# Kernel tuning notes

Hardware: AMD Instinct MI355X
Metric: run time of the kernel (lower is better)

## Reference

```python
import jax, jax.numpy as jnp
import numpy as np

N, T = 512, 48
VOCAB, EMBED, HIDDEN, IMG_DIM = 32000, 1024, 1024, 4096


def setup_inputs() -> dict:
    key = jax.random.key(0)
    ks = jax.random.split(key, 12)
    s = 0.02
    return {
        "questions": jax.random.randint(ks[0], (N, T), 0, VOCAB, dtype=jnp.int32),
        "img_features": jax.random.normal(ks[1], (N, IMG_DIM), dtype=jnp.float32),
        "emb": jax.random.normal(ks[2], (VOCAB, EMBED), dtype=jnp.float32) * s,
        "W_img": jax.random.normal(ks[3], (HIDDEN, IMG_DIM), dtype=jnp.float32) * s,
        "b_img": jnp.zeros((HIDDEN,), dtype=jnp.float32),
        "W_ih": jax.random.normal(ks[4], (4 * HIDDEN, EMBED), dtype=jnp.float32) * s,
        "W_hh": jax.random.normal(ks[5], (4 * HIDDEN, HIDDEN), dtype=jnp.float32) * s,
        "b_ih": jnp.zeros((4 * HIDDEN,), dtype=jnp.float32),
        "b_hh": jnp.zeros((4 * HIDDEN,), dtype=jnp.float32),
        "W_out": jax.random.normal(ks[6], (VOCAB, HIDDEN), dtype=jnp.float32) * s,
        "b_out": jnp.zeros((VOCAB,), dtype=jnp.float32),
        "first_words": 1,
    }


def reference(questions, img_features, emb, W_img, b_img, W_ih, W_hh, b_ih, b_hh,
              W_out, b_out, first_words):
    H = W_hh.shape[1]
    n = questions.shape[0]
    emb_q = emb[questions].transpose(1, 0, 2)          # [T, N, E]
    emb_i = img_features @ W_img.T + b_img             # [N, H]
    if first_words:
        seq = jnp.concatenate([emb_i[None], emb_q], axis=0)   # [T+1, N, E]
    else:
        seq = jnp.concatenate([emb_q, emb_i[None]], axis=0)

    def cell(carry, x_t):
        h, c = carry
        gates = x_t @ W_ih.T + b_ih + h @ W_hh.T + b_hh   # [N, 4H]
        i, f, g, o = jnp.split(gates, 4, axis=-1)          # torch LSTMCell gate order
        i, f, o = jax.nn.sigmoid(i), jax.nn.sigmoid(f), jax.nn.sigmoid(o)
        g = jnp.tanh(g)
        c = f * c + i * g
        h = o * jnp.tanh(c)
        return (h, c), h

    h0 = jnp.zeros((n, H), dtype=seq.dtype)
    (_, _), hs = jax.lax.scan(cell, (h0, h0), seq)     # hs: [T+1, N, H]
    hidden_states = hs.transpose(1, 0, 2)              # [N, T+1, H]
    output = hidden_states[:, -1, :] @ W_out.T + b_out  # [N, vocab]
    return output, hidden_states
```

## Files before the change

kernel.cpp:

```cpp
#include <hip/hip_runtime.h>
#include <hip/hip_bf16.h>
#include <stdint.h>

typedef __bf16 bf16_t;
typedef __attribute__((ext_vector_type(8))) __bf16 bf16x8;
typedef __attribute__((ext_vector_type(4))) __bf16 bf16x4;
typedef __attribute__((ext_vector_type(4))) float f32x4;
#define LL long long

__device__ __forceinline__ void gl_lds16(const bf16_t* g, bf16_t* s) {
  __builtin_amdgcn_global_load_lds(
      (const __attribute__((address_space(1))) void*)g,
      (__attribute__((address_space(3))) void*)s, 16, 0, 0);
}

__device__ __forceinline__ float sigm(float x) {
  return 1.0f / (1.0f + __expf(-x));
}
__device__ __forceinline__ float tanh_s(float x) {
  float e = __expf(-2.0f * fabsf(x));
  float t = (1.0f - e) / (1.0f + e);
  return copysignf(t, x);
}

template<int BM, int OUTBF>
__global__ __launch_bounds__(256, 2)
void gemm_bt(const bf16_t* __restrict__ A, const bf16_t* __restrict__ B,
             const float* __restrict__ bias,
             bf16_t* __restrict__ Cb, float* __restrict__ Cf,
             int N, int K, const int* __restrict__ fw, LL off0, LL off1) {
  __shared__ bf16_t lds_a[BM * 32];
  __shared__ bf16_t lds_b[128 * 32];
  const int tid = threadIdx.x;
  const int w = tid >> 6, l = tid & 63;
  const LL m0 = (LL)blockIdx.x * BM;
  const LL n0 = (LL)blockIdx.y * 128;
  constexpr int MI = BM / 32;
  const int wm = w & 1, wn = w >> 1;
  f32x4 acc[MI][4] = {};

  const int srow = l >> 2;
  const int scol = (l & 3) * 8;

  for (int kt = 0; kt < K; kt += 32) {
    for (int c = w; c < BM / 16; c += 4)
      gl_lds16(A + (m0 + c * 16 + srow) * K + kt + scol, &lds_a[c * 512]);
#pragma unroll
    for (int j = 0; j < 2; ++j) {
      int c = w * 2 + j;
      gl_lds16(B + (n0 + c * 16 + srow) * K + kt + scol, &lds_b[c * 512]);
    }
    __syncthreads();
    const int fr = l & 15, fk = (l >> 4) * 8;
    bf16x8 af[MI], bfr[4];
#pragma unroll
    for (int i = 0; i < MI; ++i)
      af[i] = *(const bf16x8*)&lds_a[(wm * (BM / 2) + i * 16 + fr) * 32 + fk];
#pragma unroll
    for (int j = 0; j < 4; ++j)
      bfr[j] = *(const bf16x8*)&lds_b[(wn * 64 + j * 16 + fr) * 32 + fk];
#pragma unroll
    for (int i = 0; i < MI; ++i)
#pragma unroll
      for (int j = 0; j < 4; ++j)
        acc[i][j] = __builtin_amdgcn_mfma_f32_16x16x32_bf16(af[i], bfr[j],
                                                            acc[i][j], 0, 0, 0);
    __syncthreads();
  }

  const LL coff = (fw[0] ? off1 : off0);
  const int er = (l >> 4) * 4, ec = l & 15;
#pragma unroll
  for (int i = 0; i < MI; ++i) {
#pragma unroll
    for (int j = 0; j < 4; ++j) {
      LL mrow = m0 + wm * (BM / 2) + i * 16 + er;
      LL ncol = n0 + wn * 64 + j * 16 + ec;
      float bs = bias[ncol];
#pragma unroll
      for (int r = 0; r < 4; ++r) {
        float v = acc[i][j][r] + bs;
        if (OUTBF) Cb[coff + (mrow + r) * N + ncol] = (bf16_t)v;
        else       Cf[(mrow + r) * N + ncol] = v;
      }
    }
  }
}

__global__ __launch_bounds__(256, 2)
void lstm_step(const bf16_t* __restrict__ h_in, const bf16_t* __restrict__ Whh,
               const bf16_t* __restrict__ Gt, float* __restrict__ c,
               bf16_t* __restrict__ h_out, float* __restrict__ hid, int t) {
  __shared__ bf16_t lds_a[64 * 32];
  __shared__ bf16_t lds_b[128 * 32];
  __shared__ float lds_ex[64 * 128];
  const int tid = threadIdx.x;
  const int w = tid >> 6, l = tid & 63;
  const int m0 = blockIdx.x * 64;
  const int n0 = blockIdx.y * 128;
  const int wm = w & 1, wn = w >> 1;
  f32x4 acc[2][4] = {};
  const int srow = l >> 2, scol = (l & 3) * 8;

  for (int kt = 0; kt < 1024; kt += 32) {
    gl_lds16(h_in + (LL)(m0 + w * 16 + srow) * 1024 + kt + scol,
             &lds_a[w * 512]);
#pragma unroll
    for (int j = 0; j < 2; ++j) {
      int ch = w * 2 + j;
      gl_lds16(Whh + (LL)(n0 + ch * 16 + srow) * 1024 + kt + scol,
               &lds_b[ch * 512]);
    }
    __syncthreads();
    const int fr = l & 15, fk = (l >> 4) * 8;
    bf16x8 af[2], bfr[4];
#pragma unroll
    for (int i = 0; i < 2; ++i)
      af[i] = *(const bf16x8*)&lds_a[(wm * 32 + i * 16 + fr) * 32 + fk];
#pragma unroll
    for (int j = 0; j < 4; ++j)
      bfr[j] = *(const bf16x8*)&lds_b[(wn * 64 + j * 16 + fr) * 32 + fk];
#pragma unroll
    for (int i = 0; i < 2; ++i)
#pragma unroll
      for (int j = 0; j < 4; ++j)
        acc[i][j] = __builtin_amdgcn_mfma_f32_16x16x32_bf16(af[i], bfr[j],
                                                            acc[i][j], 0, 0, 0);
    __syncthreads();
  }

  const int er = (l >> 4) * 4, ec = l & 15;
#pragma unroll
  for (int i = 0; i < 2; ++i)
#pragma unroll
    for (int j = 0; j < 4; ++j)
#pragma unroll
      for (int r = 0; r < 4; ++r)
        lds_ex[(wm * 32 + i * 16 + er + r) * 128 + wn * 64 + j * 16 + ec] =
            acc[i][j][r];
  __syncthreads();

  for (int cidx = tid; cidx < 2048; cidx += 256) {
    int ml = cidx >> 5, jl = cidx & 31;
    int m = m0 + ml;
    int j = (n0 >> 2) + jl;
    float4 ge = *(const float4*)&lds_ex[ml * 128 + jl * 4];
    bf16x4 g4 = *(const bf16x4*)(Gt + (LL)m * 4096 + n0 + jl * 4);
    float gi = ge.x + (float)g4[0];
    float gf = ge.y + (float)g4[1];
    float gg = ge.z + (float)g4[2];
    float go = ge.w + (float)g4[3];
    float iv = sigm(gi), fv = sigm(gf), gv = tanh_s(gg), ov = sigm(go);
    LL cij = (LL)m * 1024 + j;
    float cn = fv * c[cij] + iv * gv;
    float hn = ov * tanh_s(cn);
    c[cij] = cn;
    h_out[cij] = (bf16_t)hn;
    hid[((LL)m * 49 + t) * 1024 + j] = hn;
  }
}

__global__ __launch_bounds__(256)
void cvt_f2b(const float* __restrict__ src, bf16_t* __restrict__ dst, LL n4) {
  LL i = (LL)blockIdx.x * blockDim.x + threadIdx.x;
  LL stride = (LL)gridDim.x * blockDim.x;
  for (; i < n4; i += stride) {
    float4 v = *(const float4*)(src + i * 4);
    bf16x4 o;
    o[0] = (bf16_t)v.x; o[1] = (bf16_t)v.y; o[2] = (bf16_t)v.z; o[3] = (bf16_t)v.w;
    *(bf16x4*)(dst + i * 4) = o;
  }
}

__global__ __launch_bounds__(256)
void permute_w(const float* __restrict__ W, bf16_t* __restrict__ Wp) {
  int p = blockIdx.x;
  int r = (p & 3) * 1024 + (p >> 2);
  float4 v = *(const float4*)(W + (LL)r * 1024 + threadIdx.x * 4);
  bf16x4 o;
  o[0] = (bf16_t)v.x; o[1] = (bf16_t)v.y; o[2] = (bf16_t)v.z; o[3] = (bf16_t)v.w;
  *(bf16x4*)(Wp + (LL)p * 1024 + threadIdx.x * 4) = o;
}

__global__ __launch_bounds__(256)
void bias_comb(const float* __restrict__ bih, const float* __restrict__ bhh,
               float* __restrict__ bp) {
  int p = blockIdx.x * blockDim.x + threadIdx.x;
  int r = (p & 3) * 1024 + (p >> 2);
  bp[p] = bih[r] + bhh[r];
}

__global__ __launch_bounds__(256)
void gather_emb(const int* __restrict__ q, const float* __restrict__ emb,
                bf16_t* __restrict__ Xb, const int* __restrict__ fw) {
  int b = blockIdx.x;
  int tq = b >> 9;
  int n = b & 511;
  int slot = fw[0] ? tq + 1 : tq;
  int row = q[n * 48 + tq];
  float4 v = *(const float4*)(emb + (LL)row * 1024 + threadIdx.x * 4);
  bf16x4 o;
  o[0] = (bf16_t)v.x; o[1] = (bf16_t)v.y; o[2] = (bf16_t)v.z; o[3] = (bf16_t)v.w;
  *(bf16x4*)(Xb + ((LL)slot * 512 + n) * 1024 + threadIdx.x * 4) = o;
}

extern "C" void kernel_launch(void* const* d_in, const int* in_sizes, int n_in,
                              void* d_out, int out_size, void* d_ws,
                              size_t ws_size, hipStream_t stream) {
  const int*   questions = (const int*)  d_in[0];
  const float* img       = (const float*)d_in[1];
  const float* emb       = (const float*)d_in[2];
  const float* W_img     = (const float*)d_in[3];
  const float* b_img     = (const float*)d_in[4];
  const float* W_ih      = (const float*)d_in[5];
  const float* W_hh      = (const float*)d_in[6];
  const float* b_ih      = (const float*)d_in[7];
  const float* b_hh      = (const float*)d_in[8];
  const float* W_out     = (const float*)d_in[9];
  const float* b_out     = (const float*)d_in[10];
  const int*   fw        = (const int*)  d_in[11];

  char* ws = (char*)d_ws;
  size_t off = 0;
  auto alloc = [&](size_t bytes) {
    char* p = ws + off;
    off += (bytes + 255) & ~(size_t)255;
    return p;
  };
  bf16_t* Xb    = (bf16_t*)alloc((size_t)49 * 512 * 1024 * 2);
  bf16_t* G     = (bf16_t*)alloc((size_t)49 * 512 * 4096 * 2);
  bf16_t* Wp_ih = (bf16_t*)alloc((size_t)4096 * 1024 * 2);
  bf16_t* Wp_hh = (bf16_t*)alloc((size_t)4096 * 1024 * 2);
  bf16_t* Woutb = (bf16_t*)alloc((size_t)32000 * 1024 * 2);
  bf16_t* Wimgb = (bf16_t*)alloc((size_t)1024 * 4096 * 2);
  bf16_t* imgb  = (bf16_t*)alloc((size_t)512 * 4096 * 2);
  float*  biasp = (float*) alloc((size_t)4096 * 4);
  bf16_t* h0    = (bf16_t*)alloc((size_t)512 * 1024 * 2);
  bf16_t* h1    = (bf16_t*)alloc((size_t)512 * 1024 * 2);
  float*  cbuf  = (float*) alloc((size_t)512 * 1024 * 4);

  float* out0 = (float*)d_out;
  float* hid  = out0 + (size_t)512 * 32000;

  hipMemsetAsync(h0, 0, (size_t)512 * 1024 * 2, stream);
  hipMemsetAsync(cbuf, 0, (size_t)512 * 1024 * 4, stream);

  cvt_f2b<<<dim3(2048), dim3(256), 0, stream>>>(W_out, Woutb, (LL)32000 * 1024 / 4);
  cvt_f2b<<<dim3(1024), dim3(256), 0, stream>>>(W_img, Wimgb, (LL)1024 * 4096 / 4);
  cvt_f2b<<<dim3(512),  dim3(256), 0, stream>>>(img,   imgb,  (LL)512 * 4096 / 4);
  permute_w<<<dim3(4096), dim3(256), 0, stream>>>(W_ih, Wp_ih);
  permute_w<<<dim3(4096), dim3(256), 0, stream>>>(W_hh, Wp_hh);
  bias_comb<<<dim3(16), dim3(256), 0, stream>>>(b_ih, b_hh, biasp);
  gather_emb<<<dim3(48 * 512), dim3(256), 0, stream>>>(questions, emb, Xb, fw);

  gemm_bt<64, 1><<<dim3(8, 8), dim3(256), 0, stream>>>(
      imgb, Wimgb, b_img, Xb, nullptr, 1024, 4096, fw,
      (LL)48 * 512 * 1024, (LL)0);

  gemm_bt<128, 1><<<dim3(196, 32), dim3(256), 0, stream>>>(
      Xb, Wp_ih, biasp, G, nullptr, 4096, 1024, fw, 0, 0);

  for (int t = 0; t < 49; ++t) {
    const bf16_t* hin = (t & 1) ? h1 : h0;
    bf16_t* hout = (t & 1) ? h0 : h1;
    lstm_step<<<dim3(8, 32), dim3(256), 0, stream>>>(
        hin, Wp_hh, G + (LL)t * 512 * 4096, cbuf, hout, hid, t);
  }

  gemm_bt<128, 0><<<dim3(4, 250), dim3(256), 0, stream>>>(
      h1, Woutb, b_out, nullptr, out0, 32000, 1024, fw, 0, 0);
}
```

Before: 1.919 ms.

## Replace per-step LSTM launches with persistent kernel holding W_hh slices in LDS

The 49 separate lstm_step launches become one persistent kernel with a 64x4 grid. Each block keeps a 16-unit slice of all four gates of W_hh resident in 128KB of swizzled LDS and holds the cell state in registers. Timesteps are separated by a per-row-tile atomic counter barrier. This removes launch overhead, the per-step reload of W_hh, and the global round trips for c, but it needs all 256 blocks co-resident (otherwise the spin barrier deadlocks) and it serialises on the cross-block barrier.

```diff
diff --git a/kernel.cpp b/kernel.cpp
--- a/kernel.cpp
+++ b/kernel.cpp
@@ -6,6 +6,7 @@
 typedef __attribute__((ext_vector_type(8))) __bf16 bf16x8;
 typedef __attribute__((ext_vector_type(4))) __bf16 bf16x4;
 typedef __attribute__((ext_vector_type(4))) float f32x4;
+typedef __attribute__((ext_vector_type(16))) float f32x16;
 #define LL long long
 
 __device__ __forceinline__ void gl_lds16(const bf16_t* g, bf16_t* s) {
@@ -87,76 +88,100 @@
   }
 }
 
-__global__ __launch_bounds__(256, 2)
-void lstm_step(const bf16_t* __restrict__ h_in, const bf16_t* __restrict__ Whh,
-               const bf16_t* __restrict__ Gt, float* __restrict__ c,
-               bf16_t* __restrict__ h_out, float* __restrict__ hid, int t) {
-  __shared__ bf16_t lds_a[64 * 32];
-  __shared__ bf16_t lds_b[128 * 32];
-  __shared__ float lds_ex[64 * 128];
-  const int tid = threadIdx.x;
-  const int w = tid >> 6, l = tid & 63;
-  const int m0 = blockIdx.x * 64;
-  const int n0 = blockIdx.y * 128;
-  const int wm = w & 1, wn = w >> 1;
-  f32x4 acc[2][4] = {};
-  const int srow = l >> 2, scol = (l & 3) * 8;
-
-  for (int kt = 0; kt < 1024; kt += 32) {
-    gl_lds16(h_in + (LL)(m0 + w * 16 + srow) * 1024 + kt + scol,
-             &lds_a[w * 512]);
-#pragma unroll
-    for (int j = 0; j < 2; ++j) {
-      int ch = w * 2 + j;
-      gl_lds16(Whh + (LL)(n0 + ch * 16 + srow) * 1024 + kt + scol,
-               &lds_b[ch * 512]);
-    }
-    __syncthreads();
-    const int fr = l & 15, fk = (l >> 4) * 8;
-    bf16x8 af[2], bfr[4];
-#pragma unroll
-    for (int i = 0; i < 2; ++i)
-      af[i] = *(const bf16x8*)&lds_a[(wm * 32 + i * 16 + fr) * 32 + fk];
-#pragma unroll
-    for (int j = 0; j < 4; ++j)
-      bfr[j] = *(const bf16x8*)&lds_b[(wn * 64 + j * 16 + fr) * 32 + fk];
-#pragma unroll
-    for (int i = 0; i < 2; ++i)
-#pragma unroll
-      for (int j = 0; j < 4; ++j)
-        acc[i][j] = __builtin_amdgcn_mfma_f32_16x16x32_bf16(af[i], bfr[j],
-                                                            acc[i][j], 0, 0, 0);
-    __syncthreads();
-  }
-
-  const int er = (l >> 4) * 4, ec = l & 15;
-#pragma unroll
-  for (int i = 0; i < 2; ++i)
-#pragma unroll
-    for (int j = 0; j < 4; ++j)
-#pragma unroll
-      for (int r = 0; r < 4; ++r)
-        lds_ex[(wm * 32 + i * 16 + er + r) * 128 + wn * 64 + j * 16 + ec] =
-            acc[i][j][r];
+__global__ __launch_bounds__(256, 1)
+void lstm_persist(const bf16_t* __restrict__ Whhb, const bf16_t* __restrict__ G,
+                  bf16_t* hb0, bf16_t* hb1,
+                  float* __restrict__ hid, int* cnt) {
+  __shared__ bf16_t lds_b[64 * 1024];
+  const int tid = threadIdx.x, w = tid >> 6, l = tid & 63;
+  const int j0 = blockIdx.x * 16;
+  const int mt = blockIdx.y;
+  const int m0 = mt * 128;
+
+  for (int i = tid; i < 8192; i += 256) {
+    int ct = i >> 7, kb = i & 127;
+    int srow = (ct >> 4) * 1024 + j0 + (ct & 15);
+    bf16x8 v = *(const bf16x8*)(Whhb + (LL)srow * 1024 + kb * 8);
+    *(bf16x8*)&lds_b[ct * 1024 + ((kb ^ (ct & 7)) << 3)] = v;
+  }
   __syncthreads();
 
-  for (int cidx = tid; cidx < 2048; cidx += 256) {
-    int ml = cidx >> 5, jl = cidx & 31;
-    int m = m0 + ml;
-    int j = (n0 >> 2) + jl;
-    float4 ge = *(const float4*)&lds_ex[ml * 128 + jl * 4];
-    bf16x4 g4 = *(const bf16x4*)(Gt + (LL)m * 4096 + n0 + jl * 4);
-    float gi = ge.x + (float)g4[0];
-    float gf = ge.y + (float)g4[1];
-    float gg = ge.z + (float)g4[2];
-    float go = ge.w + (float)g4[3];
-    float iv = sigm(gi), fv = sigm(gf), gv = tanh_s(gg), ov = sigm(go);
-    LL cij = (LL)m * 1024 + j;
-    float cn = fv * c[cij] + iv * gv;
-    float hn = ov * tanh_s(cn);
-    c[cij] = cn;
-    h_out[cij] = (bf16_t)hn;
-    hid[((LL)m * 49 + t) * 1024 + j] = hn;
+  const int cc = l & 31, kh = l >> 5;
+  const int ga = cc >> 4;
+  const int unit = j0 + (cc & 15);
+  const int sw = cc & 7;
+  float creg[8];
+#pragma unroll
+  for (int r = 0; r < 8; ++r) creg[r] = 0.f;
+
+  bf16_t* hbuf[2] = {hb0, hb1};
+
+  for (int t = 0; t < 49; ++t) {
+    f32x16 acA = {}, acB = {}, acC = {}, acD = {};
+    if (t > 0) {
+      const bf16_t* hin = hbuf[(t - 1) & 1];
+      const bf16_t* ap = hin + (LL)(m0 + w * 32 + cc) * 1024 + kh * 8;
+      const bf16_t* b0p = &lds_b[cc * 1024];
+      const bf16_t* b1p = &lds_b[(cc + 32) * 1024];
+#pragma unroll 8
+      for (int kc = 0; kc < 64; ++kc) {
+        bf16x8 av = *(const bf16x8*)(ap + kc * 16);
+        int kb = (kc * 2 + kh) ^ sw;
+        bf16x8 b0 = *(const bf16x8*)(b0p + (kb << 3));
+        bf16x8 b1 = *(const bf16x8*)(b1p + (kb << 3));
+        if (kc & 1) {
+          acB = __builtin_amdgcn_mfma_f32_32x32x16_bf16(av, b0, acB, 0, 0, 0);
+          acD = __builtin_amdgcn_mfma_f32_32x32x16_bf16(av, b1, acD, 0, 0, 0);
+        } else {
+          acA = __builtin_amdgcn_mfma_f32_32x32x16_bf16(av, b0, acA, 0, 0, 0);
+          acC = __builtin_amdgcn_mfma_f32_32x32x16_bf16(av, b1, acC, 0, 0, 0);
+        }
+      }
+    }
+
+    float v0[16], v1[16], s0[16], s1[16];
+#pragma unroll
+    for (int r = 0; r < 16; ++r) {
+      v0[r] = acA[r] + acB[r];
+      v1[r] = acC[r] + acD[r];
+      s0[r] = __shfl_xor(v0[r], 16);
+      s1[r] = __shfl_xor(v1[r], 16);
+    }
+
+    const bf16_t* Gt = G + (LL)t * 512 * 4096;
+    bf16_t* hw = hbuf[t & 1];
+#pragma unroll
+    for (int rr = 0; rr < 8; ++rr) {
+      int reg = ga * 8 + rr;
+      int row = (reg & 3) + 8 * (reg >> 2) + 4 * kh;
+      LL m = m0 + w * 32 + row;
+      float gi = ga ? s0[reg] : v0[reg];
+      float gf = ga ? v0[reg] : s0[reg];
+      float gg = ga ? s1[reg] : v1[reg];
+      float go = ga ? v1[reg] : s1[reg];
+      bf16x4 gq = *(const bf16x4*)(Gt + m * 4096 + 4 * unit);
+      gi += (float)gq[0]; gf += (float)gq[1];
+      gg += (float)gq[2]; go += (float)gq[3];
+      float iv = sigm(gi), fv = sigm(gf), gv = tanh_s(gg), ov = sigm(go);
+      float cn = fv * creg[rr] + iv * gv;
+      creg[rr] = cn;
+      float hn = ov * tanh_s(cn);
+      hw[m * 1024 + unit] = (bf16_t)hn;
+      hid[(m * 49 + t) * 1024 + unit] = hn;
+    }
+
+    if (t < 48) {
+      __threadfence();
+      __syncthreads();
+      if (tid == 0) {
+        int* p = cnt + t * 4 + mt;
+        __hip_atomic_fetch_add(p, 1, __ATOMIC_RELEASE, __HIP_MEMORY_SCOPE_AGENT);
+        while (__hip_atomic_load(p, __ATOMIC_ACQUIRE,
+                                 __HIP_MEMORY_SCOPE_AGENT) < 64) {}
+      }
+      __syncthreads();
+      __threadfence();
+    }
   }
 }
 
@@ -230,26 +255,25 @@
   bf16_t* Xb    = (bf16_t*)alloc((size_t)49 * 512 * 1024 * 2);
   bf16_t* G     = (bf16_t*)alloc((size_t)49 * 512 * 4096 * 2);
   bf16_t* Wp_ih = (bf16_t*)alloc((size_t)4096 * 1024 * 2);
-  bf16_t* Wp_hh = (bf16_t*)alloc((size_t)4096 * 1024 * 2);
+  bf16_t* Whhb  = (bf16_t*)alloc((size_t)4096 * 1024 * 2);
   bf16_t* Woutb = (bf16_t*)alloc((size_t)32000 * 1024 * 2);
   bf16_t* Wimgb = (bf16_t*)alloc((size_t)1024 * 4096 * 2);
   bf16_t* imgb  = (bf16_t*)alloc((size_t)512 * 4096 * 2);
   float*  biasp = (float*) alloc((size_t)4096 * 4);
-  bf16_t* h0    = (bf16_t*)alloc((size_t)512 * 1024 * 2);
-  bf16_t* h1    = (bf16_t*)alloc((size_t)512 * 1024 * 2);
-  float*  cbuf  = (float*) alloc((size_t)512 * 1024 * 4);
+  bf16_t* hb0   = (bf16_t*)alloc((size_t)512 * 1024 * 2);
+  bf16_t* hb1   = (bf16_t*)alloc((size_t)512 * 1024 * 2);
+  int*    cnt   = (int*)   alloc((size_t)49 * 4 * 4);
 
   float* out0 = (float*)d_out;
   float* hid  = out0 + (size_t)512 * 32000;
 
-  hipMemsetAsync(h0, 0, (size_t)512 * 1024 * 2, stream);
-  hipMemsetAsync(cbuf, 0, (size_t)512 * 1024 * 4, stream);
+  hipMemsetAsync(cnt, 0, (size_t)49 * 4 * 4, stream);
 
   cvt_f2b<<<dim3(2048), dim3(256), 0, stream>>>(W_out, Woutb, (LL)32000 * 1024 / 4);
   cvt_f2b<<<dim3(1024), dim3(256), 0, stream>>>(W_img, Wimgb, (LL)1024 * 4096 / 4);
   cvt_f2b<<<dim3(512),  dim3(256), 0, stream>>>(img,   imgb,  (LL)512 * 4096 / 4);
+  cvt_f2b<<<dim3(1024), dim3(256), 0, stream>>>(W_hh,  Whhb,  (LL)4096 * 1024 / 4);
   permute_w<<<dim3(4096), dim3(256), 0, stream>>>(W_ih, Wp_ih);
-  permute_w<<<dim3(4096), dim3(256), 0, stream>>>(W_hh, Wp_hh);
   bias_comb<<<dim3(16), dim3(256), 0, stream>>>(b_ih, b_hh, biasp);
   gather_emb<<<dim3(48 * 512), dim3(256), 0, stream>>>(questions, emb, Xb, fw);
 
@@ -260,13 +284,8 @@
   gemm_bt<128, 1><<<dim3(196, 32), dim3(256), 0, stream>>>(
       Xb, Wp_ih, biasp, G, nullptr, 4096, 1024, fw, 0, 0);
 
-  for (int t = 0; t < 49; ++t) {
-    const bf16_t* hin = (t & 1) ? h1 : h0;
-    bf16_t* hout = (t & 1) ? h0 : h1;
-    lstm_step<<<dim3(8, 32), dim3(256), 0, stream>>>(
-        hin, Wp_hh, G + (LL)t * 512 * 4096, cbuf, hout, hid, t);
-  }
+  lstm_persist<<<dim3(64, 4), dim3(256), 0, stream>>>(Whhb, G, hb0, hb1, hid, cnt);
 
   gemm_bt<128, 0><<<dim3(4, 250), dim3(256), 0, stream>>>(
-      h1, Woutb, b_out, nullptr, out0, 32000, 1024, fw, 0, 0);
-}
+      hb0, Woutb, b_out, nullptr, out0, 32000, 1024, fw, 0, 0);
+}
```

Result: slower. 5.839 ms (+204.3%).
